# Optimization experiments

Measured on AMD Instinct MI355X. Metric: run time of the kernel, lower is better.

Reference implementation:

```python
import jax, jax.numpy as jnp
import numpy as np

N_NODES = 50000
N_EDGES = 800000
IN_FEATS = 128
HID = 64
HEADS = 4
ACTIONS = 16
NEG_SLOPE = 0.2  # DGL GATConv default


def setup_inputs() -> dict:
    key = jax.random.key(0)
    ks = jax.random.split(key, 14)
    s = 0.02
    return {
        "node_features": jax.random.normal(ks[0], (N_NODES, IN_FEATS), jnp.float32),
        "src": jax.random.randint(ks[1], (N_EDGES,), 0, N_NODES, jnp.int32),
        "dst": jax.random.randint(ks[2], (N_EDGES,), 0, N_NODES, jnp.int32),
        # GAT params (DGL GATConv: fc has no bias, attn_l/attn_r vectors, output bias)
        "fc_w": jax.random.normal(ks[3], (IN_FEATS, HEADS * HID), jnp.float32) * s,
        "attn_l": jax.random.normal(ks[4], (HEADS, HID), jnp.float32) * s,
        "attn_r": jax.random.normal(ks[5], (HEADS, HID), jnp.float32) * s,
        "gat_bias": jnp.zeros((HEADS * HID,), jnp.float32),
        # actor MLP: (2*H*D -> HID -> ACTIONS)
        "a_w1": jax.random.normal(ks[6], (2 * HEADS * HID, HID), jnp.float32) * s,
        "a_b1": jnp.zeros((HID,), jnp.float32),
        "a_w2": jax.random.normal(ks[7], (HID, ACTIONS), jnp.float32) * s,
        "a_b2": jnp.zeros((ACTIONS,), jnp.float32),
        # critic MLP: (H*D -> HID -> 1)
        "c_w1": jax.random.normal(ks[8], (HEADS * HID, HID), jnp.float32) * s,
        "c_b1": jnp.zeros((HID,), jnp.float32),
        "c_w2": jax.random.normal(ks[9], (HID, 1), jnp.float32) * s,
        "c_b2": jnp.zeros((1,), jnp.float32),
    }


def _gat_layer(x, src, dst, fc_w, attn_l, attn_r, gat_bias):
    # dropout layers are identity at eval time
    h = (x @ fc_w).reshape(-1, HEADS, HID)                     # [N, H, D]
    el = jnp.einsum("nhd,hd->nh", h, attn_l)                   # [N, H]
    er = jnp.einsum("nhd,hd->nh", h, attn_r)                   # [N, H]
    e = jax.nn.leaky_relu(el[src] + er[dst], NEG_SLOPE)        # [E, H]
    # segment softmax over incoming edges of each dst node
    m = jax.ops.segment_max(e, dst, num_segments=N_NODES)      # [N, H]
    ex = jnp.exp(e - m[dst])                                   # [E, H]
    z = jax.ops.segment_sum(ex, dst, num_segments=N_NODES)     # [N, H]
    alpha = ex / z[dst]                                        # [E, H]
    msg = alpha[:, :, None] * h[src]                           # [E, H, D]
    rst = jax.ops.segment_sum(msg, dst, num_segments=N_NODES)  # [N, H, D]
    rst = rst + gat_bias.reshape(1, HEADS, HID)
    return jax.nn.elu(rst)                                     # activation=F.elu


def reference(node_features, src, dst, fc_w, attn_l, attn_r, gat_bias,
              a_w1, a_b1, a_w2, a_b2, c_w1, c_b1, c_w2, c_b2):
    h = _gat_layer(node_features, src, dst, fc_w, attn_l, attn_r, gat_bias)
    h = h.reshape(-1, HEADS * HID)                             # [N, H*D]
    # per-edge src||dst concat -> actor MLP
    edge_feat = jnp.concatenate([h[src], h[dst]], axis=1)      # [E, 2*H*D]
    edge_logits = jax.nn.relu(edge_feat @ a_w1 + a_b1) @ a_w2 + a_b2
    # mean pool nodes -> critic MLP -> scalar
    graph_rep = h.mean(axis=0, keepdims=True)                  # [1, H*D]
    state_value = (jax.nn.relu(graph_rep @ c_w1 + c_b1) @ c_w2 + c_b2).mean()
    return edge_logits, state_value
```

## Files before the change

kernel.cpp:

```cpp
#include <hip/hip_runtime.h>

#define NN 50000
#define NE 800000
#define INF 128
#define HID 64
#define HEADS 4
#define HD 256
#define ACT 16
#define NEG_SLOPE 0.2f

typedef short bf8 __attribute__((ext_vector_type(8)));
typedef float f4 __attribute__((ext_vector_type(4)));
typedef unsigned short u16;

__device__ __forceinline__ u16 f2bf(float f) {
    unsigned u = __builtin_bit_cast(unsigned, f);
    u += 0x7fffu + ((u >> 16) & 1u);
    return (u16)(u >> 16);
}
__device__ __forceinline__ float bf2f(u16 h) {
    return __builtin_bit_cast(float, (unsigned)h << 16);
}


__device__ __forceinline__ void convw_body(int bid, const float* __restrict__ fc_w,
    const float* __restrict__ a_w1, const float* __restrict__ a_w2,
    u16* __restrict__ Bsw1, u16* __restrict__ Bsw2, u16* __restrict__ w2sw)
{
    const int idx = bid * 256 + threadIdx.x;
    if (idx < 32768) {
        int j = idx & 7, l = (idx >> 3) & 63, q = idx >> 9;
        int kc = q & 3, ct = q >> 2;
        int k = kc * 32 + ((l >> 4) << 3) + j, col = (ct << 4) + (l & 15);
        Bsw1[idx] = f2bf(fc_w[k * 256 + col]);
    } else if (idx < 65536) {
        int o = idx - 32768;
        int j = o & 7, l = (o >> 3) & 63, q = o >> 9;
        int kc = q & 7, ct = q >> 3;
        int k = kc * 32 + ((l >> 4) << 3) + j, col = (ct << 4) + (l & 15);
        float v = (col < 64) ? a_w1[k * 64 + col] : a_w1[(256 + k) * 64 + (col - 64)];
        Bsw2[o] = f2bf(v);
    } else if (idx < 66560) {
        int o = idx - 65536;
        int j = o & 7, l = (o >> 3) & 63, kc = o >> 9;
        int k = kc * 32 + ((l >> 4) << 3) + j, col = l & 15;
        w2sw[o] = f2bf(a_w2[k * 16 + col]);
    }
}

__device__ __forceinline__ void deg_body(int bid, const int* __restrict__ dst,
                                         int* __restrict__ deg)
{
    const int e = bid * 256 + threadIdx.x;
    if (e < NE) atomicAdd(&deg[dst[e]], 1);
}

__device__ __forceinline__ void gemm1_body(int bid, const float* __restrict__ x,
    const u16* __restrict__ Bsw, const float* __restrict__ attn_l,
    const float* __restrict__ attn_r, u16* __restrict__ hb, float* __restrict__ elr)
{
    const int tid = threadIdx.x, w = tid >> 6, l = tid & 63;
    const int lk = l >> 4;
    const int row = bid * 64 + w * 16 + (l & 15);
    const int arow = row < NN ? row : NN - 1;
    const float* ap = x + (size_t)arow * INF + lk * 8;
    bf8 a[4];
#pragma unroll
    for (int kc = 0; kc < 4; ++kc) {
        float4 f0 = *(const float4*)(ap + kc * 32);
        float4 f1 = *(const float4*)(ap + kc * 32 + 4);
        bf8 t;
        t[0] = (short)f2bf(f0.x); t[1] = (short)f2bf(f0.y);
        t[2] = (short)f2bf(f0.z); t[3] = (short)f2bf(f0.w);
        t[4] = (short)f2bf(f1.x); t[5] = (short)f2bf(f1.y);
        t[6] = (short)f2bf(f1.z); t[7] = (short)f2bf(f1.w);
        a[kc] = t;
    }
    const bool ok = row < NN;
    float elp[4] = {0.f, 0.f, 0.f, 0.f}, erp[4] = {0.f, 0.f, 0.f, 0.f};
#pragma unroll
    for (int ct = 0; ct < 16; ct += 2) {
        f4 acc0 = {0.f, 0.f, 0.f, 0.f}, acc1 = {0.f, 0.f, 0.f, 0.f};
#pragma unroll
        for (int kc = 0; kc < 4; ++kc) {
            bf8 b0 = *(const bf8*)(Bsw + (((ct * 4 + kc) * 64 + l) << 3));
            bf8 b1 = *(const bf8*)(Bsw + ((((ct + 1) * 4 + kc) * 64 + l) << 3));
            acc0 = __builtin_amdgcn_mfma_f32_16x16x32_bf16(b0, a[kc], acc0, 0, 0, 0);
            acc1 = __builtin_amdgcn_mfma_f32_16x16x32_bf16(b1, a[kc], acc1, 0, 0, 0);
        }
        const u16 r00 = f2bf(acc0[0]), r01 = f2bf(acc0[1]);
        const u16 r02 = f2bf(acc0[2]), r03 = f2bf(acc0[3]);
        const u16 r10 = f2bf(acc1[0]), r11 = f2bf(acc1[1]);
        const u16 r12 = f2bf(acc1[2]), r13 = f2bf(acc1[3]);
        if (ok) {
            *(uint2*)(hb + (size_t)row * HD + ct * 16 + lk * 4) =
                make_uint2((unsigned)r00 | ((unsigned)r01 << 16),
                           (unsigned)r02 | ((unsigned)r03 << 16));
            *(uint2*)(hb + (size_t)row * HD + (ct + 1) * 16 + lk * 4) =
                make_uint2((unsigned)r10 | ((unsigned)r11 << 16),
                           (unsigned)r12 | ((unsigned)r13 << 16));
        }
        const int hh = ct >> 2;
        const float4 al0 = *(const float4*)(attn_l + ct * 16 + lk * 4);
        const float4 al1 = *(const float4*)(attn_l + (ct + 1) * 16 + lk * 4);
        const float4 ar0 = *(const float4*)(attn_r + ct * 16 + lk * 4);
        const float4 ar1 = *(const float4*)(attn_r + (ct + 1) * 16 + lk * 4);
        const float v00 = bf2f(r00), v01 = bf2f(r01), v02 = bf2f(r02), v03 = bf2f(r03);
        const float v10 = bf2f(r10), v11 = bf2f(r11), v12 = bf2f(r12), v13 = bf2f(r13);
        elp[hh] += v00 * al0.x + v01 * al0.y + v02 * al0.z + v03 * al0.w
                 + v10 * al1.x + v11 * al1.y + v12 * al1.z + v13 * al1.w;
        erp[hh] += v00 * ar0.x + v01 * ar0.y + v02 * ar0.z + v03 * ar0.w
                 + v10 * ar1.x + v11 * ar1.y + v12 * ar1.z + v13 * ar1.w;
    }
#pragma unroll
    for (int h = 0; h < 4; ++h) {
        elp[h] += __shfl_xor(elp[h], 16); elp[h] += __shfl_xor(elp[h], 32);
        erp[h] += __shfl_xor(erp[h], 16); erp[h] += __shfl_xor(erp[h], 32);
    }
    if (ok && lk == 0) {
        *(float4*)(elr + (size_t)row * 8)     = make_float4(elp[0], elp[1], elp[2], elp[3]);
        *(float4*)(elr + (size_t)row * 8 + 4) = make_float4(erp[0], erp[1], erp[2], erp[3]);
    }
}

__device__ __forceinline__ void scatter_body(int bid, const int* __restrict__ src,
    const int* __restrict__ dst, int* __restrict__ wptr, int4* __restrict__ epack)
{
    const int e = bid * 256 + threadIdx.x;
    if (e < NE) {
        const int d = dst[e];
        const int p = atomicAdd(&wptr[d], 1);
        epack[p] = make_int4(src[e], d, e, 0);
    }
}

__device__ __forceinline__ void gemm2_body(int bid, const u16* __restrict__ rstb,
    const u16* __restrict__ Bsw, const float* __restrict__ a_b1, u16* __restrict__ pqb)
{
    const int tid = threadIdx.x, w = tid >> 6, l = tid & 63;
    const int lk = l >> 4;
    const int row = bid * 64 + w * 16 + (l & 15);
    const int arow = row < NN ? row : NN - 1;
    const u16* ap = rstb + (size_t)arow * HD + lk * 8;
    bf8 a[8];
#pragma unroll
    for (int kc = 0; kc < 8; ++kc) a[kc] = *(const bf8*)(ap + kc * 32);
    const bool ok = row < NN;
#pragma unroll
    for (int ct = 0; ct < 8; ct += 2) {
        f4 acc0 = {0.f, 0.f, 0.f, 0.f}, acc1 = {0.f, 0.f, 0.f, 0.f};
#pragma unroll
        for (int kc = 0; kc < 8; ++kc) {
            bf8 b0 = *(const bf8*)(Bsw + (((ct * 8 + kc) * 64 + l) << 3));
            bf8 b1 = *(const bf8*)(Bsw + ((((ct + 1) * 8 + kc) * 64 + l) << 3));
            acc0 = __builtin_amdgcn_mfma_f32_16x16x32_bf16(b0, a[kc], acc0, 0, 0, 0);
            acc1 = __builtin_amdgcn_mfma_f32_16x16x32_bf16(b1, a[kc], acc1, 0, 0, 0);
        }
        if (ok) {
            const int c0 = ct * 16 + lk * 4;
            float v0[4] = {acc0[0], acc0[1], acc0[2], acc0[3]};
            float v1[4] = {acc1[0], acc1[1], acc1[2], acc1[3]};
            if (c0 >= 64) {
                float4 b = *(const float4*)(a_b1 + c0 - 64);
                v0[0] += b.x; v0[1] += b.y; v0[2] += b.z; v0[3] += b.w;
            }
            if (c0 + 16 >= 64) {
                float4 b = *(const float4*)(a_b1 + c0 + 16 - 64);
                v1[0] += b.x; v1[1] += b.y; v1[2] += b.z; v1[3] += b.w;
            }
            *(uint2*)(pqb + (size_t)row * 128 + c0) =
                make_uint2((unsigned)f2bf(v0[0]) | ((unsigned)f2bf(v0[1]) << 16),
                           (unsigned)f2bf(v0[2]) | ((unsigned)f2bf(v0[3]) << 16));
            *(uint2*)(pqb + (size_t)row * 128 + c0 + 16) =
                make_uint2((unsigned)f2bf(v1[0]) | ((unsigned)f2bf(v1[1]) << 16),
                           (unsigned)f2bf(v1[2]) | ((unsigned)f2bf(v1[3]) << 16));
        }
    }
}

__device__ __forceinline__ void mean_part_body(int mb, const u16* __restrict__ rstb,
                                               float* __restrict__ part)
{
    __shared__ float lds[8][256];
    const int t = threadIdx.x, g = t >> 5, f0 = (t & 31) * 8;
    float s[8] = {};
    for (int n = mb * 8 + g; n < NN; n += 128 * 8) {
        const uint4 u = *(const uint4*)(rstb + (size_t)n * HD + f0);
        s[0] += bf2f((u16)u.x); s[1] += bf2f((u16)(u.x >> 16));
        s[2] += bf2f((u16)u.y); s[3] += bf2f((u16)(u.y >> 16));
        s[4] += bf2f((u16)u.z); s[5] += bf2f((u16)(u.z >> 16));
        s[6] += bf2f((u16)u.w); s[7] += bf2f((u16)(u.w >> 16));
    }
#pragma unroll
    for (int j = 0; j < 8; ++j) lds[g][f0 + j] = s[j];
    __syncthreads();
    float tot = 0.f;
#pragma unroll
    for (int g2 = 0; g2 < 8; ++g2) tot += lds[g2][t];
    part[(size_t)mb * 256 + t] = tot;
}

__device__ __forceinline__ void mean_fin_body(const float* __restrict__ part,
                                              float* __restrict__ gacc)
{
    const int t = threadIdx.x;
    float s = 0.f;
    for (int b = 0; b < 128; ++b) s += part[(size_t)b * 256 + t];
    gacc[t] = s;
}

__device__ __forceinline__ void edge_mlp_body(int bid, const int4* __restrict__ epack,
    const u16* __restrict__ pq, const u16* __restrict__ w2sw,
    const float* __restrict__ a_b2, float* __restrict__ out)
{
    const int tid = threadIdx.x, w = tid >> 6, l = tid & 63;
    const int lk = l >> 4;
    const int pos = bid * 64 + w * 16 + (l & 15);
    const int4 ed = epack[pos];
    const int s = ed.x, d = ed.y, e = ed.z;
    bf8 tf[2];
#pragma unroll
    for (int kc = 0; kc < 2; ++kc) {
        const int f = kc * 32 + lk * 8;
        bf8 pu = *(const bf8*)(pq + (size_t)s * 128 + f);
        bf8 qu = *(const bf8*)(pq + (size_t)d * 128 + 64 + f);
        bf8 t;
#pragma unroll
        for (int j = 0; j < 8; ++j) {
            float v = bf2f((u16)pu[j]) + bf2f((u16)qu[j]);
            v = fmaxf(v, 0.f);
            t[j] = (short)f2bf(v);
        }
        tf[kc] = t;
    }
    const float4 b2v = *(const float4*)(a_b2 + lk * 4);
    f4 acc = {b2v.x, b2v.y, b2v.z, b2v.w};
    const bf8 w0 = *(const bf8*)(w2sw + (l << 3));
    const bf8 w1 = *(const bf8*)(w2sw + ((64 + l) << 3));
    acc = __builtin_amdgcn_mfma_f32_16x16x32_bf16(w0, tf[0], acc, 0, 0, 0);
    acc = __builtin_amdgcn_mfma_f32_16x16x32_bf16(w1, tf[1], acc, 0, 0, 0);
    __builtin_nontemporal_store(acc, (f4*)(out + (size_t)e * 16 + lk * 4));
}


__global__ __launch_bounds__(256) void k_setup(const int* __restrict__ dst,
    int* __restrict__ deg, const float* __restrict__ fc_w,
    const float* __restrict__ a_w1, const float* __restrict__ a_w2,
    u16* __restrict__ Bsw1, u16* __restrict__ Bsw2, u16* __restrict__ w2sw)
{
    if (blockIdx.x < 3125) deg_body(blockIdx.x, dst, deg);
    else convw_body(blockIdx.x - 3125, fc_w, a_w1, a_w2, Bsw1, Bsw2, w2sw);
}

__global__ __launch_bounds__(256) void scan_block_kernel(const int* __restrict__ deg,
    int* __restrict__ excl, int* __restrict__ blocksum)
{
    __shared__ int tmp[256];
    const int t = threadIdx.x;
    const int i = blockIdx.x * 256 + t;
    const int v = (i < NN) ? deg[i] : 0;
    tmp[t] = v;
    __syncthreads();
    for (int off = 1; off < 256; off <<= 1) {
        int x = (t >= off) ? tmp[t - off] : 0;
        __syncthreads();
        tmp[t] += x;
        __syncthreads();
    }
    if (i < NN) excl[i] = tmp[t] - v;
    if (t == 255) blocksum[blockIdx.x] = tmp[255];
}

__global__ __launch_bounds__(256) void scan_add_kernel(const int* __restrict__ excl,
    const int* __restrict__ blocksum, int* __restrict__ rowptr, int* __restrict__ wptr)
{
    __shared__ int offs;
    const int t = threadIdx.x;
    if (t < 64) {
        int acc = 0;
        for (int i = t; i < blockIdx.x; i += 64) acc += blocksum[i];
#pragma unroll
        for (int o = 32; o; o >>= 1) acc += __shfl_xor(acc, o);
        if (t == 0) offs = acc;
    }
    __syncthreads();
    const int i = blockIdx.x * 256 + t;
    if (i < NN) {
        const int v = excl[i] + offs;
        rowptr[i] = v;
        wptr[i] = v;
    }
    if (i == 0) rowptr[NN] = NE;
}

__global__ __launch_bounds__(256) void k_g1scat(const float* __restrict__ x,
    const u16* __restrict__ Bsw1, const float* __restrict__ attn_l,
    const float* __restrict__ attn_r, u16* __restrict__ hb, float* __restrict__ elr,
    const int* __restrict__ src, const int* __restrict__ dst,
    int* __restrict__ wptr, int4* __restrict__ epack)
{
    if (blockIdx.x < 782) gemm1_body(blockIdx.x, x, Bsw1, attn_l, attn_r, hb, elr);
    else scatter_body(blockIdx.x - 782, src, dst, wptr, epack);
}

__global__ __launch_bounds__(256) void aggregate_kernel(
    const int* __restrict__ rowptr, const int4* __restrict__ epack,
    const float* __restrict__ elr, const u16* __restrict__ hb,
    const float* __restrict__ gat_bias, u16* __restrict__ rstb)
{
    __shared__ float exs[4][4][32];
    __shared__ int ssrc[4][32];
    const int w = threadIdx.x >> 6, l = threadIdx.x & 63;
    const int d = blockIdx.x * 4 + w;
    const int start = rowptr[d], end = rowptr[d + 1];
    const int h4 = l >> 4;
    const int j0 = l >> 2, ph = l & 3;
    const float erd = elr[(size_t)d * 8 + 4 + ph];
    float acc0 = 0.f, acc1 = 0.f, acc2 = 0.f, acc3 = 0.f, zsum = 0.f;
    for (int cs = start; cs < end; cs += 32) {
        const int n = min(32, end - cs);
        __builtin_amdgcn_wave_barrier();
        if (j0 < n) {
            const int s = epack[cs + j0].x;
            if (ph == 0) ssrc[w][j0] = s;
            float xv = elr[(size_t)s * 8 + ph] + erd;
            xv = xv > 0.f ? xv : NEG_SLOPE * xv;
            exs[w][ph][j0] = __expf(xv);
        }
        if (j0 + 16 < n) {
            const int s = epack[cs + j0 + 16].x;
            if (ph == 0) ssrc[w][j0 + 16] = s;
            float xv = elr[(size_t)s * 8 + ph] + erd;
            xv = xv > 0.f ? xv : NEG_SLOPE * xv;
            exs[w][ph][j0 + 16] = __expf(xv);
        }
        __builtin_amdgcn_wave_barrier();
        int jj = 0;
        for (; jj + 8 <= n; jj += 8) {
            float ev[8]; int sv[8]; uint2 uu[8];
            *(f4*)&ev[0] = *(const f4*)&exs[w][h4][jj];
            *(f4*)&ev[4] = *(const f4*)&exs[w][h4][jj + 4];
            *(int4*)&sv[0] = *(const int4*)&ssrc[w][jj];
            *(int4*)&sv[4] = *(const int4*)&ssrc[w][jj + 4];
#pragma unroll
            for (int q = 0; q < 8; ++q) {
                const int s = __builtin_amdgcn_readfirstlane(sv[q]);
                uu[q] = *(const uint2*)(hb + (size_t)s * HD + l * 4);
            }
#pragma unroll
            for (int q = 0; q < 8; ++q) {
                zsum += ev[q];
                acc0 += ev[q] * bf2f((u16)uu[q].x);
                acc1 += ev[q] * bf2f((u16)(uu[q].x >> 16));
                acc2 += ev[q] * bf2f((u16)uu[q].y);
                acc3 += ev[q] * bf2f((u16)(uu[q].y >> 16));
            }
        }
        for (; jj < n; ++jj) {
            const float e = exs[w][h4][jj];
            const int s2 = __builtin_amdgcn_readfirstlane(ssrc[w][jj]);
            const uint2 u = *(const uint2*)(hb + (size_t)s2 * HD + l * 4);
            zsum += e;
            acc0 += e * bf2f((u16)u.x);
            acc1 += e * bf2f((u16)(u.x >> 16));
            acc2 += e * bf2f((u16)u.y);
            acc3 += e * bf2f((u16)(u.y >> 16));
        }
    }
    const float inv = (end > start) ? 1.f / zsum : 0.f;
    const float4 gb = *(const float4*)(gat_bias + l * 4);
    float v0 = acc0 * inv + gb.x;
    float v1 = acc1 * inv + gb.y;
    float v2 = acc2 * inv + gb.z;
    float v3 = acc3 * inv + gb.w;
    v0 = v0 > 0.f ? v0 : (__expf(v0) - 1.f);
    v1 = v1 > 0.f ? v1 : (__expf(v1) - 1.f);
    v2 = v2 > 0.f ? v2 : (__expf(v2) - 1.f);
    v3 = v3 > 0.f ? v3 : (__expf(v3) - 1.f);
    *(uint2*)(rstb + (size_t)d * HD + l * 4) =
        make_uint2((unsigned)f2bf(v0) | ((unsigned)f2bf(v1) << 16),
                   (unsigned)f2bf(v2) | ((unsigned)f2bf(v3) << 16));
}

__global__ __launch_bounds__(256) void k_g2mean(const u16* __restrict__ rstb,
    const u16* __restrict__ Bsw2, const float* __restrict__ a_b1,
    u16* __restrict__ pqb, float* __restrict__ part)
{
    if (blockIdx.x < 782) gemm2_body(blockIdx.x, rstb, Bsw2, a_b1, pqb);
    else mean_part_body(blockIdx.x - 782, rstb, part);
}

__global__ __launch_bounds__(256) void k_mlpfin(const int4* __restrict__ epack,
    const u16* __restrict__ pqb, const u16* __restrict__ w2sw,
    const float* __restrict__ a_b2, float* __restrict__ out,
    const float* __restrict__ part, float* __restrict__ gacc)
{
    if (blockIdx.x < 12500) edge_mlp_body(blockIdx.x, epack, pqb, w2sw, a_b2, out);
    else mean_fin_body(part, gacc);
}

__global__ __launch_bounds__(256) void critic_kernel(const float* __restrict__ gacc,
    const float* __restrict__ c_w1, const float* __restrict__ c_b1,
    const float* __restrict__ c_w2, const float* __restrict__ c_b2,
    float* __restrict__ out)
{
    __shared__ float g[HD];
    __shared__ float t1[HID];
    const int t = threadIdx.x;
    g[t] = gacc[t] * (1.0f / (float)NN);
    __syncthreads();
    if (t < HID) {
        float s = c_b1[t];
        for (int c = 0; c < HD; ++c) s += g[c] * c_w1[c * HID + t];
        t1[t] = fmaxf(s, 0.f);
    }
    __syncthreads();
    if (t == 0) {
        float s = c_b2[0];
        for (int j = 0; j < HID; ++j) s += t1[j] * c_w2[j];
        out[0] = s;
    }
}

extern "C" void kernel_launch(void* const* d_in, const int* in_sizes, int n_in,
                              void* d_out, int out_size, void* d_ws, size_t ws_size,
                              hipStream_t stream)
{
    const float* x      = (const float*)d_in[0];
    const int*   src    = (const int*)d_in[1];
    const int*   dst    = (const int*)d_in[2];
    const float* fc_w   = (const float*)d_in[3];
    const float* attn_l = (const float*)d_in[4];
    const float* attn_r = (const float*)d_in[5];
    const float* gat_b  = (const float*)d_in[6];
    const float* a_w1   = (const float*)d_in[7];
    const float* a_b1   = (const float*)d_in[8];
    const float* a_w2   = (const float*)d_in[9];
    const float* a_b2   = (const float*)d_in[10];
    const float* c_w1   = (const float*)d_in[11];
    const float* c_b1   = (const float*)d_in[12];
    const float* c_w2   = (const float*)d_in[13];
    const float* c_b2   = (const float*)d_in[14];
    float* out = (float*)d_out;

    char* p = (char*)d_ws;
    u16* hb     = (u16*)p;   p += (size_t)NN * HD * 2;
    u16* rstb   = (u16*)p;   p += (size_t)NN * HD * 2;
    u16* pqb    = (u16*)p;   p += (size_t)NN * 128 * 2;
    float* elr  = (float*)p; p += (size_t)NN * 8 * 4;
    float* gacc = (float*)p; p += 1024;
    float* part = (float*)p; p += 128 * 256 * 4;
    u16* Bsw1   = (u16*)p;   p += 65536;
    u16* Bsw2   = (u16*)p;   p += 65536;
    u16* w2sw   = (u16*)p;   p += 2048;
    int* deg      = (int*)p; p += (size_t)NN * 4;
    int* excl     = (int*)p; p += (size_t)NN * 4;
    int* blocksum = (int*)p; p += 1024;
    int* rowptr   = (int*)p; p += (size_t)(NN + 4) * 4;
    int* wptr     = (int*)p; p += (size_t)NN * 4;
    int4* epack   = (int4*)p; p += (size_t)NE * 16;

    hipMemsetAsync(deg, 0, (size_t)NN * 4, stream);

    dim3 blk(256);
    const int NB = (NN + 255) / 256;
    k_setup<<<dim3(3125 + 260), blk, 0, stream>>>(dst, deg, fc_w, a_w1, a_w2,
                                                  Bsw1, Bsw2, w2sw);
    scan_block_kernel<<<dim3(NB), blk, 0, stream>>>(deg, excl, blocksum);
    scan_add_kernel<<<dim3(NB), blk, 0, stream>>>(excl, blocksum, rowptr, wptr);
    k_g1scat<<<dim3(782 + 3125), blk, 0, stream>>>(x, Bsw1, attn_l, attn_r, hb, elr,
                                                   src, dst, wptr, epack);
    aggregate_kernel<<<dim3(NN / 4), blk, 0, stream>>>(rowptr, epack, elr, hb, gat_b, rstb);
    k_g2mean<<<dim3(782 + 128), blk, 0, stream>>>(rstb, Bsw2, a_b1, pqb, part);
    k_mlpfin<<<dim3(12500 + 1), blk, 0, stream>>>(epack, pqb, w2sw, a_b2, out, part, gacc);
    critic_kernel<<<dim3(1), blk, 0, stream>>>(gacc, c_w1, c_b1, c_w2, c_b2,
                                               out + (size_t)NE * ACT);
}
```

Measured before the change: 232.2 us.

## Pack edge records into int2 and split gemm1 from the CSR scatter

Edge records shrink from int4 to int2 by packing the 16-bit source and destination ids into one word, with the edge id in the other. This halves edge-record traffic in the scatter, aggregate and edge-MLP kernels. The fused gemm1+scatter launch becomes two kernels, and gemm1 now uses 32-row blocks where each wave handles half the output columns, giving more blocks and less work per wave. It relies on the node count fitting in 16 bits and adds one kernel launch.

```diff
diff --git a/kernel.cpp b/kernel.cpp
--- a/kernel.cpp
+++ b/kernel.cpp
@@ -55,85 +55,6 @@
     if (e < NE) atomicAdd(&deg[dst[e]], 1);
 }
 
-__device__ __forceinline__ void gemm1_body(int bid, const float* __restrict__ x,
-    const u16* __restrict__ Bsw, const float* __restrict__ attn_l,
-    const float* __restrict__ attn_r, u16* __restrict__ hb, float* __restrict__ elr)
-{
-    const int tid = threadIdx.x, w = tid >> 6, l = tid & 63;
-    const int lk = l >> 4;
-    const int row = bid * 64 + w * 16 + (l & 15);
-    const int arow = row < NN ? row : NN - 1;
-    const float* ap = x + (size_t)arow * INF + lk * 8;
-    bf8 a[4];
-#pragma unroll
-    for (int kc = 0; kc < 4; ++kc) {
-        float4 f0 = *(const float4*)(ap + kc * 32);
-        float4 f1 = *(const float4*)(ap + kc * 32 + 4);
-        bf8 t;
-        t[0] = (short)f2bf(f0.x); t[1] = (short)f2bf(f0.y);
-        t[2] = (short)f2bf(f0.z); t[3] = (short)f2bf(f0.w);
-        t[4] = (short)f2bf(f1.x); t[5] = (short)f2bf(f1.y);
-        t[6] = (short)f2bf(f1.z); t[7] = (short)f2bf(f1.w);
-        a[kc] = t;
-    }
-    const bool ok = row < NN;
-    float elp[4] = {0.f, 0.f, 0.f, 0.f}, erp[4] = {0.f, 0.f, 0.f, 0.f};
-#pragma unroll
-    for (int ct = 0; ct < 16; ct += 2) {
-        f4 acc0 = {0.f, 0.f, 0.f, 0.f}, acc1 = {0.f, 0.f, 0.f, 0.f};
-#pragma unroll
-        for (int kc = 0; kc < 4; ++kc) {
-            bf8 b0 = *(const bf8*)(Bsw + (((ct * 4 + kc) * 64 + l) << 3));
-            bf8 b1 = *(const bf8*)(Bsw + ((((ct + 1) * 4 + kc) * 64 + l) << 3));
-            acc0 = __builtin_amdgcn_mfma_f32_16x16x32_bf16(b0, a[kc], acc0, 0, 0, 0);
-            acc1 = __builtin_amdgcn_mfma_f32_16x16x32_bf16(b1, a[kc], acc1, 0, 0, 0);
-        }
-        const u16 r00 = f2bf(acc0[0]), r01 = f2bf(acc0[1]);
-        const u16 r02 = f2bf(acc0[2]), r03 = f2bf(acc0[3]);
-        const u16 r10 = f2bf(acc1[0]), r11 = f2bf(acc1[1]);
-        const u16 r12 = f2bf(acc1[2]), r13 = f2bf(acc1[3]);
-        if (ok) {
-            *(uint2*)(hb + (size_t)row * HD + ct * 16 + lk * 4) =
-                make_uint2((unsigned)r00 | ((unsigned)r01 << 16),
-                           (unsigned)r02 | ((unsigned)r03 << 16));
-            *(uint2*)(hb + (size_t)row * HD + (ct + 1) * 16 + lk * 4) =
-                make_uint2((unsigned)r10 | ((unsigned)r11 << 16),
-                           (unsigned)r12 | ((unsigned)r13 << 16));
-        }
-        const int hh = ct >> 2;
-        const float4 al0 = *(const float4*)(attn_l + ct * 16 + lk * 4);
-        const float4 al1 = *(const float4*)(attn_l + (ct + 1) * 16 + lk * 4);
-        const float4 ar0 = *(const float4*)(attn_r + ct * 16 + lk * 4);
-        const float4 ar1 = *(const float4*)(attn_r + (ct + 1) * 16 + lk * 4);
-        const float v00 = bf2f(r00), v01 = bf2f(r01), v02 = bf2f(r02), v03 = bf2f(r03);
-        const float v10 = bf2f(r10), v11 = bf2f(r11), v12 = bf2f(r12), v13 = bf2f(r13);
-        elp[hh] += v00 * al0.x + v01 * al0.y + v02 * al0.z + v03 * al0.w
-                 + v10 * al1.x + v11 * al1.y + v12 * al1.z + v13 * al1.w;
-        erp[hh] += v00 * ar0.x + v01 * ar0.y + v02 * ar0.z + v03 * ar0.w
-                 + v10 * ar1.x + v11 * ar1.y + v12 * ar1.z + v13 * ar1.w;
-    }
-#pragma unroll
-    for (int h = 0; h < 4; ++h) {
-        elp[h] += __shfl_xor(elp[h], 16); elp[h] += __shfl_xor(elp[h], 32);
-        erp[h] += __shfl_xor(erp[h], 16); erp[h] += __shfl_xor(erp[h], 32);
-    }
-    if (ok && lk == 0) {
-        *(float4*)(elr + (size_t)row * 8)     = make_float4(elp[0], elp[1], elp[2], elp[3]);
-        *(float4*)(elr + (size_t)row * 8 + 4) = make_float4(erp[0], erp[1], erp[2], erp[3]);
-    }
-}
-
-__device__ __forceinline__ void scatter_body(int bid, const int* __restrict__ src,
-    const int* __restrict__ dst, int* __restrict__ wptr, int4* __restrict__ epack)
-{
-    const int e = bid * 256 + threadIdx.x;
-    if (e < NE) {
-        const int d = dst[e];
-        const int p = atomicAdd(&wptr[d], 1);
-        epack[p] = make_int4(src[e], d, e, 0);
-    }
-}
-
 __device__ __forceinline__ void gemm2_body(int bid, const u16* __restrict__ rstb,
     const u16* __restrict__ Bsw, const float* __restrict__ a_b1, u16* __restrict__ pqb)
 {
@@ -209,15 +130,15 @@
     gacc[t] = s;
 }
 
-__device__ __forceinline__ void edge_mlp_body(int bid, const int4* __restrict__ epack,
+__device__ __forceinline__ void edge_mlp_body(int bid, const int2* __restrict__ epack,
     const u16* __restrict__ pq, const u16* __restrict__ w2sw,
     const float* __restrict__ a_b2, float* __restrict__ out)
 {
     const int tid = threadIdx.x, w = tid >> 6, l = tid & 63;
     const int lk = l >> 4;
     const int pos = bid * 64 + w * 16 + (l & 15);
-    const int4 ed = epack[pos];
-    const int s = ed.x, d = ed.y, e = ed.z;
+    const int2 ed = epack[pos];
+    const int s = ed.x & 0xFFFF, d = ((unsigned)ed.x) >> 16, e = ed.y;
     bf8 tf[2];
 #pragma unroll
     for (int kc = 0; kc < 2; ++kc) {
@@ -293,18 +214,89 @@
     if (i == 0) rowptr[NN] = NE;
 }
 
-__global__ __launch_bounds__(256) void k_g1scat(const float* __restrict__ x,
-    const u16* __restrict__ Bsw1, const float* __restrict__ attn_l,
-    const float* __restrict__ attn_r, u16* __restrict__ hb, float* __restrict__ elr,
-    const int* __restrict__ src, const int* __restrict__ dst,
-    int* __restrict__ wptr, int4* __restrict__ epack)
-{
-    if (blockIdx.x < 782) gemm1_body(blockIdx.x, x, Bsw1, attn_l, attn_r, hb, elr);
-    else scatter_body(blockIdx.x - 782, src, dst, wptr, epack);
+__global__ __launch_bounds__(256) void scatter_kernel(const int* __restrict__ src,
+    const int* __restrict__ dst, int* __restrict__ wptr, int2* __restrict__ epack)
+{
+    const int e = blockIdx.x * 256 + threadIdx.x;
+    if (e < NE) {
+        const int d = dst[e];
+        const int p = atomicAdd(&wptr[d], 1);
+        epack[p] = make_int2(src[e] | (d << 16), e);
+    }
+}
+
+__global__ __launch_bounds__(256) void gemm1_kernel(const float* __restrict__ x,
+    const u16* __restrict__ Bsw, const float* __restrict__ attn_l,
+    const float* __restrict__ attn_r, u16* __restrict__ hb, float* __restrict__ elr)
+{
+    const int tid = threadIdx.x, w = tid >> 6, l = tid & 63;
+    const int lk = l >> 4;
+    const int rg = w & 1, ch = w >> 1;
+    const int row = blockIdx.x * 32 + rg * 16 + (l & 15);
+    const int arow = row < NN ? row : NN - 1;
+    const float* ap = x + (size_t)arow * INF + lk * 8;
+    bf8 a[4];
+#pragma unroll
+    for (int kc = 0; kc < 4; ++kc) {
+        float4 f0 = *(const float4*)(ap + kc * 32);
+        float4 f1 = *(const float4*)(ap + kc * 32 + 4);
+        bf8 t;
+        t[0] = (short)f2bf(f0.x); t[1] = (short)f2bf(f0.y);
+        t[2] = (short)f2bf(f0.z); t[3] = (short)f2bf(f0.w);
+        t[4] = (short)f2bf(f1.x); t[5] = (short)f2bf(f1.y);
+        t[6] = (short)f2bf(f1.z); t[7] = (short)f2bf(f1.w);
+        a[kc] = t;
+    }
+    const bool ok = row < NN;
+    float elp[2] = {0.f, 0.f}, erp[2] = {0.f, 0.f};
+#pragma unroll
+    for (int ci = 0; ci < 8; ci += 2) {
+        const int ct = ch * 8 + ci;
+        f4 acc0 = {0.f, 0.f, 0.f, 0.f}, acc1 = {0.f, 0.f, 0.f, 0.f};
+#pragma unroll
+        for (int kc = 0; kc < 4; ++kc) {
+            bf8 b0 = *(const bf8*)(Bsw + (((ct * 4 + kc) * 64 + l) << 3));
+            bf8 b1 = *(const bf8*)(Bsw + ((((ct + 1) * 4 + kc) * 64 + l) << 3));
+            acc0 = __builtin_amdgcn_mfma_f32_16x16x32_bf16(b0, a[kc], acc0, 0, 0, 0);
+            acc1 = __builtin_amdgcn_mfma_f32_16x16x32_bf16(b1, a[kc], acc1, 0, 0, 0);
+        }
+        const u16 r00 = f2bf(acc0[0]), r01 = f2bf(acc0[1]);
+        const u16 r02 = f2bf(acc0[2]), r03 = f2bf(acc0[3]);
+        const u16 r10 = f2bf(acc1[0]), r11 = f2bf(acc1[1]);
+        const u16 r12 = f2bf(acc1[2]), r13 = f2bf(acc1[3]);
+        if (ok) {
+            *(uint2*)(hb + (size_t)row * HD + ct * 16 + lk * 4) =
+                make_uint2((unsigned)r00 | ((unsigned)r01 << 16),
+                           (unsigned)r02 | ((unsigned)r03 << 16));
+            *(uint2*)(hb + (size_t)row * HD + (ct + 1) * 16 + lk * 4) =
+                make_uint2((unsigned)r10 | ((unsigned)r11 << 16),
+                           (unsigned)r12 | ((unsigned)r13 << 16));
+        }
+        const int hh = ci >> 2;
+        const float4 al0 = *(const float4*)(attn_l + ct * 16 + lk * 4);
+        const float4 al1 = *(const float4*)(attn_l + (ct + 1) * 16 + lk * 4);
+        const float4 ar0 = *(const float4*)(attn_r + ct * 16 + lk * 4);
+        const float4 ar1 = *(const float4*)(attn_r + (ct + 1) * 16 + lk * 4);
+        const float v00 = bf2f(r00), v01 = bf2f(r01), v02 = bf2f(r02), v03 = bf2f(r03);
+        const float v10 = bf2f(r10), v11 = bf2f(r11), v12 = bf2f(r12), v13 = bf2f(r13);
+        elp[hh] += v00 * al0.x + v01 * al0.y + v02 * al0.z + v03 * al0.w
+                 + v10 * al1.x + v11 * al1.y + v12 * al1.z + v13 * al1.w;
+        erp[hh] += v00 * ar0.x + v01 * ar0.y + v02 * ar0.z + v03 * ar0.w
+                 + v10 * ar1.x + v11 * ar1.y + v12 * ar1.z + v13 * ar1.w;
+    }
+#pragma unroll
+    for (int h = 0; h < 2; ++h) {
+        elp[h] += __shfl_xor(elp[h], 16); elp[h] += __shfl_xor(elp[h], 32);
+        erp[h] += __shfl_xor(erp[h], 16); erp[h] += __shfl_xor(erp[h], 32);
+    }
+    if (ok && lk == 0) {
+        *(float2*)(elr + (size_t)row * 8 + ch * 2)     = make_float2(elp[0], elp[1]);
+        *(float2*)(elr + (size_t)row * 8 + 4 + ch * 2) = make_float2(erp[0], erp[1]);
+    }
 }
 
 __global__ __launch_bounds__(256) void aggregate_kernel(
-    const int* __restrict__ rowptr, const int4* __restrict__ epack,
+    const int* __restrict__ rowptr, const int2* __restrict__ epack,
     const float* __restrict__ elr, const u16* __restrict__ hb,
     const float* __restrict__ gat_bias, u16* __restrict__ rstb)
 {
@@ -321,14 +313,14 @@
         const int n = min(32, end - cs);
         __builtin_amdgcn_wave_barrier();
         if (j0 < n) {
-            const int s = epack[cs + j0].x;
+            const int s = epack[cs + j0].x & 0xFFFF;
             if (ph == 0) ssrc[w][j0] = s;
             float xv = elr[(size_t)s * 8 + ph] + erd;
             xv = xv > 0.f ? xv : NEG_SLOPE * xv;
             exs[w][ph][j0] = __expf(xv);
         }
         if (j0 + 16 < n) {
-            const int s = epack[cs + j0 + 16].x;
+            const int s = epack[cs + j0 + 16].x & 0xFFFF;
             if (ph == 0) ssrc[w][j0 + 16] = s;
             float xv = elr[(size_t)s * 8 + ph] + erd;
             xv = xv > 0.f ? xv : NEG_SLOPE * xv;
@@ -390,7 +382,7 @@
     else mean_part_body(blockIdx.x - 782, rstb, part);
 }
 
-__global__ __launch_bounds__(256) void k_mlpfin(const int4* __restrict__ epack,
+__global__ __launch_bounds__(256) void k_mlpfin(const int2* __restrict__ epack,
     const u16* __restrict__ pqb, const u16* __restrict__ w2sw,
     const float* __restrict__ a_b2, float* __restrict__ out,
     const float* __restrict__ part, float* __restrict__ gacc)
@@ -458,7 +450,7 @@
     int* blocksum = (int*)p; p += 1024;
     int* rowptr   = (int*)p; p += (size_t)(NN + 4) * 4;
     int* wptr     = (int*)p; p += (size_t)NN * 4;
-    int4* epack   = (int4*)p; p += (size_t)NE * 16;
+    int2* epack   = (int2*)p; p += (size_t)NE * 8;
 
     hipMemsetAsync(deg, 0, (size_t)NN * 4, stream);
 
@@ -468,8 +460,8 @@
                                                   Bsw1, Bsw2, w2sw);
     scan_block_kernel<<<dim3(NB), blk, 0, stream>>>(deg, excl, blocksum);
     scan_add_kernel<<<dim3(NB), blk, 0, stream>>>(excl, blocksum, rowptr, wptr);
-    k_g1scat<<<dim3(782 + 3125), blk, 0, stream>>>(x, Bsw1, attn_l, attn_r, hb, elr,
-                                                   src, dst, wptr, epack);
+    scatter_kernel<<<dim3(3125), blk, 0, stream>>>(src, dst, wptr, epack);
+    gemm1_kernel<<<dim3((NN + 31) / 32), blk, 0, stream>>>(x, Bsw1, attn_l, attn_r, hb, elr);
     aggregate_kernel<<<dim3(NN / 4), blk, 0, stream>>>(rowptr, epack, elr, hb, gat_b, rstb);
     k_g2mean<<<dim3(782 + 128), blk, 0, stream>>>(rstb, Bsw2, a_b1, pqb, part);
     k_mlpfin<<<dim3(12500 + 1), blk, 0, stream>>>(epack, pqb, w2sw, a_b2, out, part, gacc);
```

After: 243.6 us. 1.05x slower.
